# Kernel optimization log

Measured on AMD Instinct MI355X. Metric: run time of the kernel, lower is better.

## Reference

```python
import jax, jax.numpy as jnp
import numpy as np

S, P = 64, 32          # scenes, pedestrians per scene (uniform)
N = S * P              # total pedestrians = 2048
H, E = 64, 64          # h_dim, embedding_dim
D1, D2 = 512, 1024     # mlp_pre_pool hidden, bottleneck_dim
EPS = 1e-5             # torch BatchNorm1d eps


def _batchnorm(x, gamma, beta):
    # Training-mode BN with per-scene batch stats (matches the per-scene
    # loop in the original, where BN sees one scene's num_ped^2 rows).
    # x: [S, P*P, D]
    mu = jnp.mean(x, axis=1, keepdims=True)
    var = jnp.mean(jnp.square(x - mu), axis=1, keepdims=True)  # biased var, as torch BN
    return (x - mu) * jax.lax.rsqrt(var + EPS) * gamma + beta


def setup_inputs() -> dict:
    key = jax.random.key(0)
    ks = jax.random.split(key, 16)
    h_states = jax.random.normal(ks[0], (1, N, H), jnp.float32)
    starts = jnp.arange(S, dtype=jnp.int32) * P
    seq_start_end = jnp.stack([starts, starts + P], axis=1)  # [S, 2]
    end_pos = jax.random.normal(ks[1], (N, 2), jnp.float32)
    rel_pos = jax.random.normal(ks[2], (N, 2), jnp.float32)  # unused (pooling_dim=2) but a fwd arg
    sc = 0.05
    params = dict(
        W_embed=jax.random.normal(ks[3], (2, E), jnp.float32) * sc,
        b_embed=jnp.zeros((E,), jnp.float32),
        W1=jax.random.normal(ks[4], (E + H, D1), jnp.float32) * sc,
        b1=jnp.zeros((D1,), jnp.float32),
        g1=jnp.ones((D1,), jnp.float32),
        be1=jnp.zeros((D1,), jnp.float32),
        W2=jax.random.normal(ks[5], (D1, D2), jnp.float32) * sc,
        b2=jnp.zeros((D2,), jnp.float32),
        g2=jnp.ones((D2,), jnp.float32),
        be2=jnp.zeros((D2,), jnp.float32),
    )
    return dict(h_states=h_states, seq_start_end=seq_start_end,
                end_pos=end_pos, rel_pos=rel_pos, **params)


def reference(h_states, seq_start_end, end_pos, rel_pos,
              W_embed, b_embed, W1, b1, g1, be1, W2, b2, g2, be2):
    # Uniform scenes: seq_start_end delimits S contiguous blocks of P peds.
    pos = end_pos.reshape(S, P, 2)
    h = h_states.reshape(N, H).reshape(S, P, H)
    # Original indexing: row (k*P + j) -> pos[j] - pos[k], hidden[j];
    # the final view(P, P, -1).max(1) maxes over j for each k.
    rel = pos[:, None, :, :] - pos[:, :, None, :]          # [S, Pk, Pj, 2]
    emb = rel @ W_embed + b_embed                          # [S, Pk, Pj, E]
    hid = jnp.broadcast_to(h[:, None, :, :], (S, P, P, H)) # hidden of j
    x = jnp.concatenate([emb, hid], axis=-1).reshape(S, P * P, E + H)
    x = jax.nn.relu(_batchnorm(x @ W1 + b1, g1, be1))      # [S, P*P, 512]
    x = jax.nn.relu(_batchnorm(x @ W2 + b2, g2, be2))      # [S, P*P, 1024]
    pool_h = x.reshape(S, P, P, D2).max(axis=2)            # max over j
    return pool_h.reshape(N, D2)
```

## Files before the change

kernel.cpp:

```cpp
#include <hip/hip_runtime.h>
#include <hip/hip_bf16.h>

#define S_ 64
#define P_ 32
#define N_ 2048
#define H_ 64
#define E_ 64
#define D1_ 512
#define D2_ 1024
#define EPS_ 1e-5f

typedef unsigned short u16;
using bf16x8 = __attribute__((ext_vector_type(8))) __bf16;
using floatx4 = __attribute__((ext_vector_type(4))) float;

__device__ inline u16 f2bf(float x) {
    unsigned u = __float_as_uint(x);
    unsigned r = (u + 0x7fffu + ((u >> 16) & 1u)) >> 16;
    return (u16)r;
}


__device__ void prep_scene_256(int u, int tid, float* smem,
                               const float* __restrict__ pos, const float* __restrict__ h,
                               const float* __restrict__ We, const float* __restrict__ W1,
                               const float* __restrict__ g1, const float* __restrict__ be1,
                               float* __restrict__ A, float* __restrict__ Bv) {
    const int s = u >> 2, dq = u & 3;
    const int jg = tid >> 7, dl = tid & 127;
    const int d = (dq << 7) + dl;
    float* hs = smem;
    float* ps = smem + 2048;
    float* red = smem + 2112;
    for (int i = tid; i < 2048; i += 256) hs[i] = h[(size_t)s * 2048 + i];
    if (tid < 64) ps[tid] = pos[s * 64 + tid];
    __syncthreads();
    float wq0 = 0.f, wq1 = 0.f;
    for (int e = 0; e < 64; ++e) {
        const float wv = W1[e * 512 + d];
        wq0 += We[e] * wv;
        wq1 += We[64 + e] * wv;
    }
    float w[16], uu[16];
#pragma unroll
    for (int jj = 0; jj < 16; ++jj) w[jj] = 0.f;
    const float4* h4 = (const float4*)hs;
    for (int e4 = 0; e4 < 16; ++e4) {
        const float c0 = W1[(64 + e4 * 4 + 0) * 512 + d];
        const float c1 = W1[(64 + e4 * 4 + 1) * 512 + d];
        const float c2 = W1[(64 + e4 * 4 + 2) * 512 + d];
        const float c3 = W1[(64 + e4 * 4 + 3) * 512 + d];
#pragma unroll
        for (int jj = 0; jj < 16; ++jj) {
            const float4 hv = h4[((jg << 4) + jj) * 16 + e4];
            w[jj] += hv.x * c0 + hv.y * c1 + hv.z * c2 + hv.w * c3;
        }
    }
    float sw = 0.f, sww = 0.f, su = 0.f, suu = 0.f;
#pragma unroll
    for (int jj = 0; jj < 16; ++jj) {
        const int j = (jg << 4) + jj;
        uu[jj] = ps[2 * j] * wq0 + ps[2 * j + 1] * wq1;
        w[jj] += uu[jj];
        sw += w[jj]; sww += w[jj] * w[jj];
        su += uu[jj]; suu += uu[jj] * uu[jj];
    }
    red[(jg << 7) + dl] = sw;
    red[256 + (jg << 7) + dl] = sww;
    red[512 + (jg << 7) + dl] = su;
    red[768 + (jg << 7) + dl] = suu;
    __syncthreads();
    const float tw = red[dl] + red[128 + dl];
    const float tww = red[256 + dl] + red[384 + dl];
    const float tu = red[512 + dl] + red[640 + dl];
    const float tuu = red[768 + dl] + red[896 + dl];
    const float mw = tw * (1.f / 32.f), mu2 = tu * (1.f / 32.f);
    const float var = (tww * (1.f / 32.f) - mw * mw) + (tuu * (1.f / 32.f) - mu2 * mu2);
    const float sc = rsqrtf(var + EPS_) * g1[d];
    const float bb = be1[d];
#pragma unroll
    for (int jj = 0; jj < 16; ++jj) {
        const int j = (jg << 4) + jj;
        A[(size_t)(s * 32 + j) * 512 + d] = (w[jj] - mw) * sc + bb;
        Bv[(size_t)(s * 32 + j) * 512 + d] = (uu[jj] - mu2) * sc;
    }
}

__device__ void w2t_tile_256(int b2, int tid, void* smem,
                             const float* __restrict__ W2, u16* __restrict__ w2t) {
    float (*tile)[65] = (float (*)[65])smem;
    const int bi = b2 & 15, bj = b2 >> 4;
    const int tx = tid & 63, ty = tid >> 6;
#pragma unroll
    for (int i = 0; i < 64; i += 4)
        tile[ty + i][tx] = W2[(size_t)(bj * 64 + ty + i) * 1024 + bi * 64 + tx];
    __syncthreads();
#pragma unroll
    for (int i = 0; i < 64; i += 4)
        w2t[(size_t)(bi * 64 + ty + i) * 512 + bj * 64 + tx] = f2bf(tile[tx][ty + i]);
}

__global__ __launch_bounds__(256, 2)
void k_gemm(const float* __restrict__ A, const float* __restrict__ Bv,
            const u16* __restrict__ w2t,
            float* __restrict__ maxv, float* __restrict__ minv,
            float* __restrict__ psum, float* __restrict__ psumsq) {
    __shared__ __align__(16) u16 As[128 * 64];
    __shared__ __align__(16) u16 Ws[256 * 64];
    const int tid = threadIdx.x;
    const int wave = tid >> 6, lane = tid & 63;
    const int wm = wave >> 1, wn = wave & 1;
    const int quad = lane >> 4, l16 = lane & 15;
    const int lrow = lane >> 3, lchk = lane & 7;
    const int gchk = lchk ^ lrow;
    const int sj = tid >> 3, sc8 = tid & 7;
    const int mt = blockIdx.x;
    const int s2 = mt >> 3, rb = mt & 7;
    const int pedb = rb << 2;
    const float* Aj = A + ((size_t)(s2 * 32 + sj) << 9) + (sc8 << 3);
    const float* Bp = Bv + ((size_t)(s2 * 32 + pedb) << 9) + (sc8 << 3);
    const int swz = (sc8 ^ (sj & 7)) << 3;

    for (int cs = 0; cs < 4; ++cs) {
        const int N0 = cs << 8;
        floatx4 acc[4][8] = {};
        for (int it = 0; it < 8; ++it) {
            const int k0 = it << 6;
#pragma unroll
            for (int t = 0; t < 8; ++t) {
                const int rbase = (wave << 6) + (t << 3);
                const u16* gb = w2t + (size_t)(N0 + rbase + lrow) * 512 + (k0 + (gchk << 3));
                __builtin_amdgcn_global_load_lds(
                    (const __attribute__((address_space(1))) void*)gb,
                    (__attribute__((address_space(3))) void*)(Ws + (rbase << 6)), 16, 0, 0);
            }
            {
                const float4 alo = *(const float4*)(Aj + k0);
                const float4 ahi = *(const float4*)(Aj + k0 + 4);
#pragma unroll
                for (int p = 0; p < 4; ++p) {
                    const int r = (p << 5) + sj;
                    const float4 blo = *(const float4*)(Bp + ((size_t)p << 9) + k0);
                    const float4 bhi = *(const float4*)(Bp + ((size_t)p << 9) + k0 + 4);
                    bf16x8 o;
                    o[0] = (__bf16)fmaxf(alo.x - blo.x, 0.f);
                    o[1] = (__bf16)fmaxf(alo.y - blo.y, 0.f);
                    o[2] = (__bf16)fmaxf(alo.z - blo.z, 0.f);
                    o[3] = (__bf16)fmaxf(alo.w - blo.w, 0.f);
                    o[4] = (__bf16)fmaxf(ahi.x - bhi.x, 0.f);
                    o[5] = (__bf16)fmaxf(ahi.y - bhi.y, 0.f);
                    o[6] = (__bf16)fmaxf(ahi.z - bhi.z, 0.f);
                    o[7] = (__bf16)fmaxf(ahi.w - bhi.w, 0.f);
                    *(bf16x8*)(As + (r << 6) + swz) = o;
                }
            }
            __syncthreads();
#pragma unroll
            for (int kk = 0; kk < 2; ++kk) {
                const int ck = (kk << 2) + quad;
                const int po = (ck ^ (l16 & 7)) << 3;
                bf16x8 af[4], wf[8];
#pragma unroll
                for (int tm = 0; tm < 4; ++tm) {
                    const int row = (wm << 6) + (tm << 4) + l16;
                    af[tm] = *(const bf16x8*)(As + (row << 6) + po);
                }
#pragma unroll
                for (int tn = 0; tn < 8; ++tn) {
                    const int wrow = (wn << 7) + (tn << 4) + l16;
                    wf[tn] = *(const bf16x8*)(Ws + (wrow << 6) + ((ck ^ (wrow & 7)) << 3));
                }
#pragma unroll
                for (int tm = 0; tm < 4; ++tm)
#pragma unroll
                    for (int tn = 0; tn < 8; ++tn)
                        acc[tm][tn] = __builtin_amdgcn_mfma_f32_16x16x32_bf16(
                            af[tm], wf[tn], acc[tm][tn], 0, 0, 0);
            }
            __syncthreads();
        }
#pragma unroll
        for (int tn = 0; tn < 8; ++tn) {
            const int col = N0 + (wn << 7) + (tn << 4) + l16;
            float wsum = 0.f, wsq = 0.f;
#pragma unroll
            for (int gp = 0; gp < 2; ++gp) {
                float vmax = -3.4e38f, vmin = 3.4e38f, vs = 0.f, vq = 0.f;
#pragma unroll
                for (int tm = gp * 2; tm < gp * 2 + 2; ++tm)
#pragma unroll
                    for (int r = 0; r < 4; ++r) {
                        const float v = acc[tm][tn][r];
                        vmax = fmaxf(vmax, v);
                        vmin = fminf(vmin, v);
                        vs += v;
                        vq += v * v;
                    }
#pragma unroll
                for (int off = 16; off < 64; off <<= 1) {
                    vmax = fmaxf(vmax, __shfl_xor(vmax, off));
                    vmin = fminf(vmin, __shfl_xor(vmin, off));
                    vs += __shfl_xor(vs, off);
                    vq += __shfl_xor(vq, off);
                }
                if (quad == 0) {
                    const int kg = s2 * 32 + pedb + (wm << 1) + gp;
                    maxv[(size_t)kg * 1024 + col] = vmax;
                    minv[(size_t)kg * 1024 + col] = vmin;
                }
                wsum += vs;
                wsq += vq;
            }
            if (quad == 0) {
                const int slot = (s2 << 4) + (rb << 1) + wm;
                psum[(size_t)slot * 1024 + col] = wsum;
                psumsq[(size_t)slot * 1024 + col] = wsq;
            }
        }
    }
}

__global__ __launch_bounds__(256)
void k_prep(const float* __restrict__ pos, const float* __restrict__ h,
            const float* __restrict__ We, const float* __restrict__ W1,
            const float* __restrict__ g1, const float* __restrict__ be1,
            const float* __restrict__ W2,
            float* __restrict__ A, float* __restrict__ Bv, u16* __restrict__ w2t) {
    __shared__ __align__(16) char smem_raw[16912];
    const int bid = blockIdx.x;
    if (bid < 256)
        prep_scene_256(bid, threadIdx.x, (float*)smem_raw, pos, h, We, W1, g1, be1, A, Bv);
    else
        w2t_tile_256(bid - 256, threadIdx.x, smem_raw, W2, w2t);
}

__global__ __launch_bounds__(256)
void k_final(const float* __restrict__ maxv, const float* __restrict__ minv,
             const float* __restrict__ psum, const float* __restrict__ psumsq,
             const float* __restrict__ g2, const float* __restrict__ be2,
             float* __restrict__ out) {
    const int u = blockIdx.x, tid = threadIdx.x;
    const int s3 = u >> 2;
    const int c = ((u & 3) << 8) + tid;
    float sm = 0.f, sq = 0.f;
#pragma unroll
    for (int t = 0; t < 16; ++t) {
        sm += psum[(size_t)(s3 * 16 + t) * 1024 + c];
        sq += psumsq[(size_t)(s3 * 16 + t) * 1024 + c];
    }
    const float mu = sm * (1.f / 1024.f);
    const float var = sq * (1.f / 1024.f) - mu * mu;
    const float inv = rsqrtf(var + EPS_);
    const float scale = g2[c] * inv;
    const float bb = be2[c];
    const float* src = (scale >= 0.f) ? maxv : minv;
    for (int k = 0; k < 32; ++k) {
        const float v = src[(size_t)(s3 * 32 + k) * 1024 + c];
        out[(size_t)(s3 * 32 + k) * 1024 + c] = fmaxf((v - mu) * scale + bb, 0.f);
    }
}

extern "C" void kernel_launch(void* const* d_in, const int* in_sizes, int n_in,
                              void* d_out, int out_size, void* d_ws, size_t ws_size,
                              hipStream_t stream) {
    const float* h_states = (const float*)d_in[0];
    const float* end_pos = (const float*)d_in[2];
    const float* W_embed = (const float*)d_in[4];
    const float* W1 = (const float*)d_in[6];
    const float* g1 = (const float*)d_in[8];
    const float* be1 = (const float*)d_in[9];
    const float* W2 = (const float*)d_in[10];
    const float* g2 = (const float*)d_in[12];
    const float* be2 = (const float*)d_in[13];
    float* out = (float*)d_out;

    float* Abuf = (float*)d_ws;
    float* Bbuf = Abuf + 1048576;
    float* maxv = Bbuf + 1048576;
    float* minv = maxv + 2097152;
    float* psum = minv + 2097152;
    float* psumsq = psum + 1048576;
    u16* w2t = (u16*)(psumsq + 1048576);

    k_prep<<<dim3(384), dim3(256), 0, stream>>>(end_pos, h_states, W_embed, W1,
                                                g1, be1, W2, Abuf, Bbuf, w2t);
    k_gemm<<<dim3(512), dim3(256), 0, stream>>>(Abuf, Bbuf, w2t, maxv, minv, psum, psumsq);
    k_final<<<dim3(256), dim3(256), 0, stream>>>(maxv, minv, psum, psumsq, g2, be2, out);
}
```

Measured before the change: 186.3 us.

## Rewrite GEMM kernel as double-buffered 256x256 tile pipeline with 8 waves

Restructures the main GEMM into 512-thread blocks that each compute a 256x256 output tile, with double-buffered LDS (128 KB dynamic) for the A and W2 tiles. The next K-slice is loaded and the ReLU(A-B) operand is built while MFMAs run on the current buffer, split into four sub-phases with raw barriers, explicit waitcnts and s_setprio around the MFMA bursts. The grid is retiled to 1024 blocks over single N-chunks, and k_final sums 8 partial-stat slots instead of 16. The aim is to hide global-load and operand-build latency behind compute, at the cost of much higher LDS use per block (which limits occupancy) and more fragile manual synchronisation.

```diff
diff --git a/kernel.cpp b/kernel.cpp
--- a/kernel.cpp
+++ b/kernel.cpp
@@ -100,122 +100,230 @@
         w2t[(size_t)(bi * 64 + ty + i) * 512 + bj * 64 + tx] = f2bf(tile[tx][ty + i]);
 }
 
-__global__ __launch_bounds__(256, 2)
+
+__device__ __forceinline__ void ld4x4(float4 d[4], const float* __restrict__ p) {
+    d[0] = *(const float4*)(p);
+    d[1] = *(const float4*)(p + 4);
+    d[2] = *(const float4*)(p + 8);
+    d[3] = *(const float4*)(p + 12);
+}
+
+__device__ __forceinline__ void build_half(u16* __restrict__ AsN, int rowb,
+                                           int posA, int posB,
+                                           const float4 a[4], const float4 b[4]) {
+    bf16x8 o;
+    o[0] = (__bf16)fmaxf(a[0].x - b[0].x, 0.f);
+    o[1] = (__bf16)fmaxf(a[0].y - b[0].y, 0.f);
+    o[2] = (__bf16)fmaxf(a[0].z - b[0].z, 0.f);
+    o[3] = (__bf16)fmaxf(a[0].w - b[0].w, 0.f);
+    o[4] = (__bf16)fmaxf(a[1].x - b[1].x, 0.f);
+    o[5] = (__bf16)fmaxf(a[1].y - b[1].y, 0.f);
+    o[6] = (__bf16)fmaxf(a[1].z - b[1].z, 0.f);
+    o[7] = (__bf16)fmaxf(a[1].w - b[1].w, 0.f);
+    *(bf16x8*)(AsN + rowb + posA) = o;
+    bf16x8 p;
+    p[0] = (__bf16)fmaxf(a[2].x - b[2].x, 0.f);
+    p[1] = (__bf16)fmaxf(a[2].y - b[2].y, 0.f);
+    p[2] = (__bf16)fmaxf(a[2].z - b[2].z, 0.f);
+    p[3] = (__bf16)fmaxf(a[2].w - b[2].w, 0.f);
+    p[4] = (__bf16)fmaxf(a[3].x - b[3].x, 0.f);
+    p[5] = (__bf16)fmaxf(a[3].y - b[3].y, 0.f);
+    p[6] = (__bf16)fmaxf(a[3].z - b[3].z, 0.f);
+    p[7] = (__bf16)fmaxf(a[3].w - b[3].w, 0.f);
+    *(bf16x8*)(AsN + rowb + posB) = p;
+}
+
+__device__ __forceinline__ void stage_ws(const u16* __restrict__ w2t, u16* WsN,
+                                         int N0, int kcol, int h, int wave,
+                                         int lrow, int gchk) {
+#pragma unroll
+    for (int c = 0; c < 2; ++c) {
+        const int rbase = h * 128 + wave * 16 + c * 8;
+        const u16* gb = w2t + (size_t)(N0 + rbase + lrow) * 512 + kcol + gchk * 8;
+        __builtin_amdgcn_global_load_lds(
+            (const __attribute__((address_space(1))) void*)gb,
+            (__attribute__((address_space(3))) void*)(WsN + rbase * 64), 16, 0, 0);
+    }
+}
+
+template <int QM, int QN>
+__device__ __forceinline__ void read_frags(bf16x8 af[4], bf16x8 wf[2],
+                                           const u16* __restrict__ Ab,
+                                           const u16* __restrict__ Wb,
+                                           int wm, int wn, int l16, int pos) {
+#pragma unroll
+    for (int i = 0; i < 4; ++i)
+        af[i] = *(const bf16x8*)(Ab + (wm * 128 + (QM * 4 + i) * 16 + l16) * 64 + pos);
+#pragma unroll
+    for (int n = 0; n < 2; ++n)
+        wf[n] = *(const bf16x8*)(Wb + (wn * 64 + (QN * 2 + n) * 16 + l16) * 64 + pos);
+}
+
+template <int QM, int QN>
+__device__ __forceinline__ void do_mfma(floatx4 (&acc)[8][4],
+                                        const bf16x8 af[4], const bf16x8 wf[2]) {
+#pragma unroll
+    for (int i = 0; i < 4; ++i)
+#pragma unroll
+        for (int n = 0; n < 2; ++n)
+            acc[QM * 4 + i][QN * 2 + n] = __builtin_amdgcn_mfma_f32_16x16x32_bf16(
+                af[i], wf[n], acc[QM * 4 + i][QN * 2 + n], 0, 0, 0);
+}
+
+#define LGKM0() asm volatile("s_waitcnt lgkmcnt(0)" ::: "memory")
+#define VM0()   asm volatile("s_waitcnt vmcnt(0)" ::: "memory")
+
+__global__ __launch_bounds__(512, 2)
 void k_gemm(const float* __restrict__ A, const float* __restrict__ Bv,
             const u16* __restrict__ w2t,
             float* __restrict__ maxv, float* __restrict__ minv,
             float* __restrict__ psum, float* __restrict__ psumsq) {
-    __shared__ __align__(16) u16 As[128 * 64];
-    __shared__ __align__(16) u16 Ws[256 * 64];
+    extern __shared__ __align__(16) char lds_raw[];
+    u16* AsB = (u16*)lds_raw;
+    u16* WsB = AsB + 32768;
+
     const int tid = threadIdx.x;
     const int wave = tid >> 6, lane = tid & 63;
-    const int wm = wave >> 1, wn = wave & 1;
+    const int wm = wave >> 2, wn = wave & 3;
     const int quad = lane >> 4, l16 = lane & 15;
-    const int lrow = lane >> 3, lchk = lane & 7;
-    const int gchk = lchk ^ lrow;
-    const int sj = tid >> 3, sc8 = tid & 7;
-    const int mt = blockIdx.x;
-    const int s2 = mt >> 3, rb = mt & 7;
-    const int pedb = rb << 2;
-    const float* Aj = A + ((size_t)(s2 * 32 + sj) << 9) + (sc8 << 3);
-    const float* Bp = Bv + ((size_t)(s2 * 32 + pedb) << 9) + (sc8 << 3);
-    const int swz = (sc8 ^ (sj & 7)) << 3;
-
-    for (int cs = 0; cs < 4; ++cs) {
-        const int N0 = cs << 8;
-        floatx4 acc[4][8] = {};
-        for (int it = 0; it < 8; ++it) {
-            const int k0 = it << 6;
-#pragma unroll
-            for (int t = 0; t < 8; ++t) {
-                const int rbase = (wave << 6) + (t << 3);
-                const u16* gb = w2t + (size_t)(N0 + rbase + lrow) * 512 + (k0 + (gchk << 3));
-                __builtin_amdgcn_global_load_lds(
-                    (const __attribute__((address_space(1))) void*)gb,
-                    (__attribute__((address_space(3))) void*)(Ws + (rbase << 6)), 16, 0, 0);
+    const int lrow = lane >> 3, gchk = (lane & 7) ^ lrow;
+
+    const int bid = blockIdx.x;
+    const int mb = bid >> 2, nb = bid & 3;
+    const int s = mb >> 2, kq = mb & 3;
+    const int N0 = nb << 8;
+
+    const int brow = tid >> 2, kq4 = tid & 3;
+    const int j0 = brow & 31, pl0 = brow >> 5;
+    const float* Arow = A + ((size_t)(s * 32 + j0) << 9) + (kq4 << 4);
+    const float* Brow0 = Bv + ((size_t)(s * 32 + kq * 8 + pl0) << 9) + (kq4 << 4);
+    const float* Brow1 = Brow0 + (4 << 9);
+    const int posA = ((kq4 * 2) ^ (brow & 7)) << 3;
+    const int posB = ((kq4 * 2 + 1) ^ (brow & 7)) << 3;
+    const int rowb0 = brow * 64;
+    const int rowb1 = (128 + brow) * 64;
+
+    const int posk0 = ((quad) ^ (l16 & 7)) << 3;
+    const int posk1 = ((4 + quad) ^ (l16 & 7)) << 3;
+
+    floatx4 acc[8][4] = {};
+
+    {
+        float4 xa[4], xb[4], yb[4];
+        ld4x4(xa, Arow); ld4x4(xb, Brow0); ld4x4(yb, Brow1);
+        stage_ws(w2t, WsB, N0, 0, 0, wave, lrow, gchk);
+        stage_ws(w2t, WsB, N0, 0, 1, wave, lrow, gchk);
+        build_half(AsB, rowb0, posA, posB, xa, xb);
+        build_half(AsB, rowb1, posA, posB, xa, yb);
+        LGKM0();
+        VM0();
+        __builtin_amdgcn_s_barrier();
+    }
+
+    for (int t = 0; t < 8; ++t) {
+        const int buf = t & 1;
+        const u16* Ab = AsB + (buf << 14);
+        const u16* Wb = WsB + (buf << 14);
+        u16* AsN = AsB + ((buf ^ 1) << 14);
+        u16* WsN = WsB + ((buf ^ 1) << 14);
+        const bool pf = (t < 7);
+        const int kn = (t + 1) << 6;
+
+        float4 xa[4], xb[4], yb[4];
+
+        {
+            bf16x8 af[4], wf[2];
+            read_frags<0, 0>(af, wf, Ab, Wb, wm, wn, l16, posk0);
+            if (pf) { ld4x4(xa, Arow + kn); ld4x4(xb, Brow0 + kn); }
+            LGKM0();
+            __builtin_amdgcn_s_barrier();
+            __builtin_amdgcn_s_setprio(1);
+            do_mfma<0, 0>(acc, af, wf);
+            read_frags<0, 0>(af, wf, Ab, Wb, wm, wn, l16, posk1);
+            do_mfma<0, 0>(acc, af, wf);
+            __builtin_amdgcn_s_setprio(0);
+        }
+        {
+            bf16x8 af[4], wf[2];
+            read_frags<0, 1>(af, wf, Ab, Wb, wm, wn, l16, posk0);
+            if (pf) {
+                stage_ws(w2t, WsN, N0, kn, 0, wave, lrow, gchk);
+                ld4x4(yb, Brow1 + kn);
+                build_half(AsN, rowb0, posA, posB, xa, xb);
             }
-            {
-                const float4 alo = *(const float4*)(Aj + k0);
-                const float4 ahi = *(const float4*)(Aj + k0 + 4);
-#pragma unroll
-                for (int p = 0; p < 4; ++p) {
-                    const int r = (p << 5) + sj;
-                    const float4 blo = *(const float4*)(Bp + ((size_t)p << 9) + k0);
-                    const float4 bhi = *(const float4*)(Bp + ((size_t)p << 9) + k0 + 4);
-                    bf16x8 o;
-                    o[0] = (__bf16)fmaxf(alo.x - blo.x, 0.f);
-                    o[1] = (__bf16)fmaxf(alo.y - blo.y, 0.f);
-                    o[2] = (__bf16)fmaxf(alo.z - blo.z, 0.f);
-                    o[3] = (__bf16)fmaxf(alo.w - blo.w, 0.f);
-                    o[4] = (__bf16)fmaxf(ahi.x - bhi.x, 0.f);
-                    o[5] = (__bf16)fmaxf(ahi.y - bhi.y, 0.f);
-                    o[6] = (__bf16)fmaxf(ahi.z - bhi.z, 0.f);
-                    o[7] = (__bf16)fmaxf(ahi.w - bhi.w, 0.f);
-                    *(bf16x8*)(As + (r << 6) + swz) = o;
+            LGKM0();
+            __builtin_amdgcn_s_barrier();
+            __builtin_amdgcn_s_setprio(1);
+            do_mfma<0, 1>(acc, af, wf);
+            read_frags<0, 1>(af, wf, Ab, Wb, wm, wn, l16, posk1);
+            do_mfma<0, 1>(acc, af, wf);
+            __builtin_amdgcn_s_setprio(0);
+        }
+        {
+            bf16x8 af[4], wf[2];
+            read_frags<1, 0>(af, wf, Ab, Wb, wm, wn, l16, posk0);
+            if (pf) {
+                stage_ws(w2t, WsN, N0, kn, 1, wave, lrow, gchk);
+                build_half(AsN, rowb1, posA, posB, xa, yb);
+            }
+            LGKM0();
+            __builtin_amdgcn_s_barrier();
+            __builtin_amdgcn_s_setprio(1);
+            do_mfma<1, 0>(acc, af, wf);
+            read_frags<1, 0>(af, wf, Ab, Wb, wm, wn, l16, posk1);
+            do_mfma<1, 0>(acc, af, wf);
+            __builtin_amdgcn_s_setprio(0);
+        }
+        {
+            bf16x8 af[4], wf[2];
+            read_frags<1, 1>(af, wf, Ab, Wb, wm, wn, l16, posk0);
+            LGKM0();
+            if (pf) VM0();
+            __builtin_amdgcn_s_barrier();
+            __builtin_amdgcn_s_setprio(1);
+            do_mfma<1, 1>(acc, af, wf);
+            read_frags<1, 1>(af, wf, Ab, Wb, wm, wn, l16, posk1);
+            do_mfma<1, 1>(acc, af, wf);
+            __builtin_amdgcn_s_setprio(0);
+        }
+    }
+
+#pragma unroll
+    for (int tn = 0; tn < 4; ++tn) {
+        const int col = N0 + wn * 64 + tn * 16 + l16;
+        float wsum = 0.f, wsq = 0.f;
+#pragma unroll
+        for (int e = 0; e < 4; ++e) {
+            float vmax = -3.4e38f, vmin = 3.4e38f, vs = 0.f, vq = 0.f;
+#pragma unroll
+            for (int tm = e * 2; tm < e * 2 + 2; ++tm)
+#pragma unroll
+                for (int r = 0; r < 4; ++r) {
+                    const float v = acc[tm][tn][r];
+                    vmax = fmaxf(vmax, v);
+                    vmin = fminf(vmin, v);
+                    vs += v;
+                    vq += v * v;
                 }
-            }
-            __syncthreads();
-#pragma unroll
-            for (int kk = 0; kk < 2; ++kk) {
-                const int ck = (kk << 2) + quad;
-                const int po = (ck ^ (l16 & 7)) << 3;
-                bf16x8 af[4], wf[8];
-#pragma unroll
-                for (int tm = 0; tm < 4; ++tm) {
-                    const int row = (wm << 6) + (tm << 4) + l16;
-                    af[tm] = *(const bf16x8*)(As + (row << 6) + po);
-                }
-#pragma unroll
-                for (int tn = 0; tn < 8; ++tn) {
-                    const int wrow = (wn << 7) + (tn << 4) + l16;
-                    wf[tn] = *(const bf16x8*)(Ws + (wrow << 6) + ((ck ^ (wrow & 7)) << 3));
-                }
-#pragma unroll
-                for (int tm = 0; tm < 4; ++tm)
-#pragma unroll
-                    for (int tn = 0; tn < 8; ++tn)
-                        acc[tm][tn] = __builtin_amdgcn_mfma_f32_16x16x32_bf16(
-                            af[tm], wf[tn], acc[tm][tn], 0, 0, 0);
-            }
-            __syncthreads();
-        }
-#pragma unroll
-        for (int tn = 0; tn < 8; ++tn) {
-            const int col = N0 + (wn << 7) + (tn << 4) + l16;
-            float wsum = 0.f, wsq = 0.f;
-#pragma unroll
-            for (int gp = 0; gp < 2; ++gp) {
-                float vmax = -3.4e38f, vmin = 3.4e38f, vs = 0.f, vq = 0.f;
-#pragma unroll
-                for (int tm = gp * 2; tm < gp * 2 + 2; ++tm)
-#pragma unroll
-                    for (int r = 0; r < 4; ++r) {
-                        const float v = acc[tm][tn][r];
-                        vmax = fmaxf(vmax, v);
-                        vmin = fminf(vmin, v);
-                        vs += v;
-                        vq += v * v;
-                    }
-#pragma unroll
-                for (int off = 16; off < 64; off <<= 1) {
-                    vmax = fmaxf(vmax, __shfl_xor(vmax, off));
-                    vmin = fminf(vmin, __shfl_xor(vmin, off));
-                    vs += __shfl_xor(vs, off);
-                    vq += __shfl_xor(vq, off);
-                }
-                if (quad == 0) {
-                    const int kg = s2 * 32 + pedb + (wm << 1) + gp;
-                    maxv[(size_t)kg * 1024 + col] = vmax;
-                    minv[(size_t)kg * 1024 + col] = vmin;
-                }
-                wsum += vs;
-                wsq += vq;
+#pragma unroll
+            for (int off = 16; off < 64; off <<= 1) {
+                vmax = fmaxf(vmax, __shfl_xor(vmax, off));
+                vmin = fminf(vmin, __shfl_xor(vmin, off));
+                vs += __shfl_xor(vs, off);
+                vq += __shfl_xor(vq, off);
             }
             if (quad == 0) {
-                const int slot = (s2 << 4) + (rb << 1) + wm;
-                psum[(size_t)slot * 1024 + col] = wsum;
-                psumsq[(size_t)slot * 1024 + col] = wsq;
+                const int kg = s * 32 + kq * 8 + wm * 4 + e;
+                maxv[(size_t)kg * 1024 + col] = vmax;
+                minv[(size_t)kg * 1024 + col] = vmin;
             }
+            wsum += vs;
+            wsq += vq;
+        }
+        if (quad == 0) {
+            const int slot = ((s * 4 + kq) << 1) + wm;
+            psum[(size_t)slot * 1024 + col] = wsum;
+            psumsq[(size_t)slot * 1024 + col] = wsq;
         }
     }
 }
@@ -244,9 +352,9 @@
     const int c = ((u & 3) << 8) + tid;
     float sm = 0.f, sq = 0.f;
 #pragma unroll
-    for (int t = 0; t < 16; ++t) {
-        sm += psum[(size_t)(s3 * 16 + t) * 1024 + c];
-        sq += psumsq[(size_t)(s3 * 16 + t) * 1024 + c];
+    for (int t = 0; t < 8; ++t) {
+        sm += psum[(size_t)(s3 * 8 + t) * 1024 + c];
+        sq += psumsq[(size_t)(s3 * 8 + t) * 1024 + c];
     }
     const float mu = sm * (1.f / 1024.f);
     const float var = sq * (1.f / 1024.f) - mu * mu;
@@ -282,8 +390,16 @@
     float* psumsq = psum + 1048576;
     u16* w2t = (u16*)(psumsq + 1048576);
 
+    static int lds_opt_in = 0;
+    if (!lds_opt_in) {
+        hipFuncSetAttribute(reinterpret_cast<const void*>(k_gemm),
+                            hipFuncAttributeMaxDynamicSharedMemorySize, 131072);
+        lds_opt_in = 1;
+    }
+
     k_prep<<<dim3(384), dim3(256), 0, stream>>>(end_pos, h_states, W_embed, W1,
                                                 g1, be1, W2, Abuf, Bbuf, w2t);
-    k_gemm<<<dim3(512), dim3(256), 0, stream>>>(Abuf, Bbuf, w2t, maxv, minv, psum, psumsq);
+    k_gemm<<<dim3(1024), dim3(512), 131072, stream>>>(Abuf, Bbuf, w2t, maxv, minv,
+                                                      psum, psumsq);
     k_final<<<dim3(256), dim3(256), 0, stream>>>(maxv, minv, psum, psumsq, g2, be2, out);
 }
```

After: 216.3 us. 1.16x slower.

## Double-buffer W2 tiles in LDS and prefetch next tile during MFMA

Applied to the files above, without the earlier changes.

Flattens the column-slab and K loops into one 32-step loop and double-buffers the weight tile in LDS, issuing async global-to-LDS loads for the next step before computing on the current one. Explicit vmcnt/lgkmcnt waits and raw barriers replace __syncthreads. This is meant to hide weight-load latency behind the matrix-core work. LDS use grows to 80KB of dynamic shared memory per block, which may reduce how many blocks fit on a CU compared with the requested two.

```diff
diff --git a/kernel.cpp b/kernel.cpp
--- a/kernel.cpp
+++ b/kernel.cpp
@@ -100,13 +100,19 @@
         w2t[(size_t)(bi * 64 + ty + i) * 512 + bj * 64 + tx] = f2bf(tile[tx][ty + i]);
 }
 
+#define LGKM0() asm volatile("s_waitcnt lgkmcnt(0)" ::: "memory")
+#define VMC8()  asm volatile("s_waitcnt vmcnt(8)" ::: "memory")
+#define VM0()   asm volatile("s_waitcnt vmcnt(0)" ::: "memory")
+
 __global__ __launch_bounds__(256, 2)
 void k_gemm(const float* __restrict__ A, const float* __restrict__ Bv,
             const u16* __restrict__ w2t,
             float* __restrict__ maxv, float* __restrict__ minv,
             float* __restrict__ psum, float* __restrict__ psumsq) {
-    __shared__ __align__(16) u16 As[128 * 64];
-    __shared__ __align__(16) u16 Ws[256 * 64];
+    extern __shared__ __align__(16) char lds_raw[];
+    u16* As = (u16*)lds_raw;
+    u16* Ws = As + 8192;
+
     const int tid = threadIdx.x;
     const int wave = tid >> 6, lane = tid & 63;
     const int wm = wave >> 1, wn = wave & 1;
@@ -121,101 +127,133 @@
     const float* Bp = Bv + ((size_t)(s2 * 32 + pedb) << 9) + (sc8 << 3);
     const int swz = (sc8 ^ (sj & 7)) << 3;
 
-    for (int cs = 0; cs < 4; ++cs) {
-        const int N0 = cs << 8;
-        floatx4 acc[4][8] = {};
-        for (int it = 0; it < 8; ++it) {
-            const int k0 = it << 6;
+    floatx4 acc[4][8] = {};
+
+    {
+#pragma unroll
+        for (int t = 0; t < 8; ++t) {
+            const int rbase = (wave << 6) + (t << 3);
+            const u16* gb = w2t + (size_t)(rbase + lrow) * 512 + (gchk << 3);
+            __builtin_amdgcn_global_load_lds(
+                (const __attribute__((address_space(1))) void*)gb,
+                (__attribute__((address_space(3))) void*)(Ws + (rbase << 6)), 16, 0, 0);
+        }
+    }
+
+    for (int u = 0; u < 32; ++u) {
+        const int cs = u >> 3, it = u & 7;
+        const int k0 = it << 6, N0 = cs << 8;
+        const int buf = u & 1;
+        const u16* Wcur = Ws + (buf << 14);
+        u16* Wnxt = Ws + ((buf ^ 1) << 14);
+
+        {
+            const float4 alo = *(const float4*)(Aj + k0);
+            const float4 ahi = *(const float4*)(Aj + k0 + 4);
+#pragma unroll
+            for (int p = 0; p < 4; ++p) {
+                const int r = (p << 5) + sj;
+                const float4 blo = *(const float4*)(Bp + ((size_t)p << 9) + k0);
+                const float4 bhi = *(const float4*)(Bp + ((size_t)p << 9) + k0 + 4);
+                bf16x8 o;
+                o[0] = (__bf16)fmaxf(alo.x - blo.x, 0.f);
+                o[1] = (__bf16)fmaxf(alo.y - blo.y, 0.f);
+                o[2] = (__bf16)fmaxf(alo.z - blo.z, 0.f);
+                o[3] = (__bf16)fmaxf(alo.w - blo.w, 0.f);
+                o[4] = (__bf16)fmaxf(ahi.x - bhi.x, 0.f);
+                o[5] = (__bf16)fmaxf(ahi.y - bhi.y, 0.f);
+                o[6] = (__bf16)fmaxf(ahi.z - bhi.z, 0.f);
+                o[7] = (__bf16)fmaxf(ahi.w - bhi.w, 0.f);
+                *(bf16x8*)(As + (r << 6) + swz) = o;
+            }
+        }
+
+        if (u < 31) {
+            const int cs1 = (u + 1) >> 3, it1 = (u + 1) & 7;
+            const int kn = it1 << 6, Nn = cs1 << 8;
 #pragma unroll
             for (int t = 0; t < 8; ++t) {
                 const int rbase = (wave << 6) + (t << 3);
-                const u16* gb = w2t + (size_t)(N0 + rbase + lrow) * 512 + (k0 + (gchk << 3));
+                const u16* gb = w2t + (size_t)(Nn + rbase + lrow) * 512 + (kn + (gchk << 3));
                 __builtin_amdgcn_global_load_lds(
                     (const __attribute__((address_space(1))) void*)gb,
-                    (__attribute__((address_space(3))) void*)(Ws + (rbase << 6)), 16, 0, 0);
-            }
-            {
-                const float4 alo = *(const float4*)(Aj + k0);
-                const float4 ahi = *(const float4*)(Aj + k0 + 4);
-#pragma unroll
-                for (int p = 0; p < 4; ++p) {
-                    const int r = (p << 5) + sj;
-                    const float4 blo = *(const float4*)(Bp + ((size_t)p << 9) + k0);
-                    const float4 bhi = *(const float4*)(Bp + ((size_t)p << 9) + k0 + 4);
-                    bf16x8 o;
-                    o[0] = (__bf16)fmaxf(alo.x - blo.x, 0.f);
-                    o[1] = (__bf16)fmaxf(alo.y - blo.y, 0.f);
-                    o[2] = (__bf16)fmaxf(alo.z - blo.z, 0.f);
-                    o[3] = (__bf16)fmaxf(alo.w - blo.w, 0.f);
-                    o[4] = (__bf16)fmaxf(ahi.x - bhi.x, 0.f);
-                    o[5] = (__bf16)fmaxf(ahi.y - bhi.y, 0.f);
-                    o[6] = (__bf16)fmaxf(ahi.z - bhi.z, 0.f);
-                    o[7] = (__bf16)fmaxf(ahi.w - bhi.w, 0.f);
-                    *(bf16x8*)(As + (r << 6) + swz) = o;
-                }
-            }
-            __syncthreads();
-#pragma unroll
-            for (int kk = 0; kk < 2; ++kk) {
-                const int ck = (kk << 2) + quad;
-                const int po = (ck ^ (l16 & 7)) << 3;
-                bf16x8 af[4], wf[8];
-#pragma unroll
-                for (int tm = 0; tm < 4; ++tm) {
-                    const int row = (wm << 6) + (tm << 4) + l16;
-                    af[tm] = *(const bf16x8*)(As + (row << 6) + po);
-                }
-#pragma unroll
-                for (int tn = 0; tn < 8; ++tn) {
-                    const int wrow = (wn << 7) + (tn << 4) + l16;
-                    wf[tn] = *(const bf16x8*)(Ws + (wrow << 6) + ((ck ^ (wrow & 7)) << 3));
-                }
-#pragma unroll
-                for (int tm = 0; tm < 4; ++tm)
-#pragma unroll
-                    for (int tn = 0; tn < 8; ++tn)
-                        acc[tm][tn] = __builtin_amdgcn_mfma_f32_16x16x32_bf16(
-                            af[tm], wf[tn], acc[tm][tn], 0, 0, 0);
-            }
-            __syncthreads();
-        }
-#pragma unroll
-        for (int tn = 0; tn < 8; ++tn) {
-            const int col = N0 + (wn << 7) + (tn << 4) + l16;
-            float wsum = 0.f, wsq = 0.f;
-#pragma unroll
-            for (int gp = 0; gp < 2; ++gp) {
-                float vmax = -3.4e38f, vmin = 3.4e38f, vs = 0.f, vq = 0.f;
-#pragma unroll
-                for (int tm = gp * 2; tm < gp * 2 + 2; ++tm)
-#pragma unroll
-                    for (int r = 0; r < 4; ++r) {
-                        const float v = acc[tm][tn][r];
-                        vmax = fmaxf(vmax, v);
-                        vmin = fminf(vmin, v);
-                        vs += v;
-                        vq += v * v;
+                    (__attribute__((address_space(3))) void*)(Wnxt + (rbase << 6)), 16, 0, 0);
+            }
+            VMC8();
+        } else {
+            VM0();
+        }
+        LGKM0();
+        __builtin_amdgcn_s_barrier();
+
+#pragma unroll
+        for (int kk = 0; kk < 2; ++kk) {
+            const int ck = (kk << 2) + quad;
+            const int po = (ck ^ (l16 & 7)) << 3;
+            bf16x8 af[4], wf[8];
+#pragma unroll
+            for (int tm = 0; tm < 4; ++tm) {
+                const int row = (wm << 6) + (tm << 4) + l16;
+                af[tm] = *(const bf16x8*)(As + (row << 6) + po);
+            }
+#pragma unroll
+            for (int tn = 0; tn < 8; ++tn) {
+                const int wrow = (wn << 7) + (tn << 4) + l16;
+                wf[tn] = *(const bf16x8*)(Wcur + (wrow << 6) + ((ck ^ (wrow & 7)) << 3));
+            }
+#pragma unroll
+            for (int tm = 0; tm < 4; ++tm)
+#pragma unroll
+                for (int tn = 0; tn < 8; ++tn)
+                    acc[tm][tn] = __builtin_amdgcn_mfma_f32_16x16x32_bf16(
+                        af[tm], wf[tn], acc[tm][tn], 0, 0, 0);
+        }
+        __builtin_amdgcn_s_barrier();
+
+        if (it == 7) {
+#pragma unroll
+            for (int tn = 0; tn < 8; ++tn) {
+                const int col = N0 + (wn << 7) + (tn << 4) + l16;
+                float wsum = 0.f, wsq = 0.f;
+#pragma unroll
+                for (int gp = 0; gp < 2; ++gp) {
+                    float vmax = -3.4e38f, vmin = 3.4e38f, vs = 0.f, vq = 0.f;
+#pragma unroll
+                    for (int tm = gp * 2; tm < gp * 2 + 2; ++tm)
+#pragma unroll
+                        for (int r = 0; r < 4; ++r) {
+                            const float v = acc[tm][tn][r];
+                            vmax = fmaxf(vmax, v);
+                            vmin = fminf(vmin, v);
+                            vs += v;
+                            vq += v * v;
+                        }
+#pragma unroll
+                    for (int off = 16; off < 64; off <<= 1) {
+                        vmax = fmaxf(vmax, __shfl_xor(vmax, off));
+                        vmin = fminf(vmin, __shfl_xor(vmin, off));
+                        vs += __shfl_xor(vs, off);
+                        vq += __shfl_xor(vq, off);
                     }
-#pragma unroll
-                for (int off = 16; off < 64; off <<= 1) {
-                    vmax = fmaxf(vmax, __shfl_xor(vmax, off));
-                    vmin = fminf(vmin, __shfl_xor(vmin, off));
-                    vs += __shfl_xor(vs, off);
-                    vq += __shfl_xor(vq, off);
+                    if (quad == 0) {
+                        const int kg = s2 * 32 + pedb + (wm << 1) + gp;
+                        maxv[(size_t)kg * 1024 + col] = vmax;
+                        minv[(size_t)kg * 1024 + col] = vmin;
+                    }
+                    wsum += vs;
+                    wsq += vq;
                 }
                 if (quad == 0) {
-                    const int kg = s2 * 32 + pedb + (wm << 1) + gp;
-                    maxv[(size_t)kg * 1024 + col] = vmax;
-                    minv[(size_t)kg * 1024 + col] = vmin;
+                    const int slot = (s2 << 4) + (rb << 1) + wm;
+                    psum[(size_t)slot * 1024 + col] = wsum;
+                    psumsq[(size_t)slot * 1024 + col] = wsq;
                 }
-                wsum += vs;
-                wsq += vq;
-            }
-            if (quad == 0) {
-                const int slot = (s2 << 4) + (rb << 1) + wm;
-                psum[(size_t)slot * 1024 + col] = wsum;
-                psumsq[(size_t)slot * 1024 + col] = wsq;
-            }
+            }
+#pragma unroll
+            for (int tm = 0; tm < 4; ++tm)
+#pragma unroll
+                for (int tn = 0; tn < 8; ++tn)
+                    acc[tm][tn] = floatx4{0.f, 0.f, 0.f, 0.f};
         }
     }
 }
@@ -282,8 +320,16 @@
     float* psumsq = psum + 1048576;
     u16* w2t = (u16*)(psumsq + 1048576);
 
+    static int lds_opt_in = 0;
+    if (!lds_opt_in) {
+        hipFuncSetAttribute(reinterpret_cast<const void*>(k_gemm),
+                            hipFuncAttributeMaxDynamicSharedMemorySize, 81920);
+        lds_opt_in = 1;
+    }
+
     k_prep<<<dim3(384), dim3(256), 0, stream>>>(end_pos, h_states, W_embed, W1,
                                                 g1, be1, W2, Abuf, Bbuf, w2t);
-    k_gemm<<<dim3(512), dim3(256), 0, stream>>>(Abuf, Bbuf, w2t, maxv, minv, psum, psumsq);
+    k_gemm<<<dim3(512), dim3(256), 81920, stream>>>(Abuf, Bbuf, w2t, maxv, minv,
+                                                    psum, psumsq);
     k_final<<<dim3(256), dim3(256), 0, stream>>>(maxv, minv, psum, psumsq, g2, be2, out);
 }
```

Measured after the change: 186.5 us. About the same (+0.1%).
